# Optimization experiments

Hardware: AMD Instinct MI355X
Metric: run time of the kernel (lower is better)

Reference implementation:

```python
import jax, jax.numpy as jnp
from jax import lax
import numpy as np

N, T, V = 32, 32, 128
C_FEAT, C_BOX, C_CLS = 256, 4, 4
C_IN = C_FEAT + C_BOX + C_CLS  # 264 (is_scene=False concatenates x,b,c)
C_OUT = 64
K = 9
EPS = 1e-3  # keras BatchNormalization default epsilon


def _bn4(x, g, b, m, v):
    # inference-mode BN over channel axis 1 of (N,C,T,V)
    s = (g * lax.rsqrt(v + EPS))[None, :, None, None]
    return (x - m[None, :, None, None]) * s + b[None, :, None, None]


def _stgcn(x, a, imp, w, bw, ga, ba, ma, va, al, wt, bt, gb, bb, mb, vb, residual):
    res = x if residual else 0.0
    # SGCN: 1x1 conv (channels_first) then adjacency aggregation; dropout is identity at inference
    h = jnp.einsum('nctv,co->notv', x, w) + bw[None, :, None, None]
    h = jnp.einsum('nctv,ntvw->nctw', h, a * imp)
    # TGCN: BN -> PReLU(alpha per (C,T,V)) -> temporal conv (K,1) SAME -> BN -> (dropout=id)
    h = _bn4(h, ga, ba, ma, va)
    h = jnp.where(h >= 0, h, al[None] * h)
    h = lax.conv_general_dilated(h, wt, (1, 1), 'SAME',
                                 dimension_numbers=('NCHW', 'HWIO', 'NCHW')) + bt[None, :, None, None]
    h = _bn4(h, gb, bb, mb, vb)
    return h + res  # use_mdn=True -> no final PReLU


def _forward(x, b, c, a, dbn_g, dbn_b, dbn_m, dbn_v,
             w0, bw0, imp0, g0a, b0a, m0a, v0a, al0, wt0, bt0, g0b, b0b, m0b, v0b,
             w1, bw1, imp1, g1a, b1a, m1a, v1a, al1, wt1, bt1, g1b, b1b, m1b, v1b):
    x = jnp.concatenate([x, b, c], axis=-1)  # (N,T,V,C_IN)
    n, t, v, cc = x.shape
    # data BN over flattened (V*C) channel axis, exactly as the TF reshapes do
    x = jnp.transpose(x, (0, 2, 3, 1)).reshape(n, v * cc, t)
    s = (dbn_g * lax.rsqrt(dbn_v + EPS))[None, :, None]
    x = (x - dbn_m[None, :, None]) * s + dbn_b[None, :, None]
    # NOTE: the original does transpose(0,1,3,2) then a *reshape* to (N,C,T,V); replicate exactly
    x = x.reshape(n, v, cc, t).transpose(0, 1, 3, 2).reshape(n, cc, t, v)
    x = _stgcn(x, a, imp0, w0, bw0, g0a, b0a, m0a, v0a, al0, wt0, bt0, g0b, b0b, m0b, v0b, residual=False)
    x = _stgcn(x, a, imp1, w1, bw1, g1a, b1a, m1a, v1a, al1, wt1, bt1, g1b, b1b, m1b, v1b, residual=True)
    x = x[:, :, :, 0]  # (N,C_OUT,T)
    return jnp.transpose(x, (0, 2, 1))  # (N,T,C_OUT)


def setup_inputs():
    key = jax.random.key(0)
    ks = jax.random.split(key, 40)
    rn = lambda k, s, sc=1.0: jax.random.normal(k, s, jnp.float32) * sc
    ru = lambda k, s, lo, hi: jax.random.uniform(k, s, jnp.float32, lo, hi)
    d = {}
    d['x'] = rn(ks[0], (N, T, V, C_FEAT))
    d['b'] = rn(ks[1], (N, T, V, C_BOX))
    d['c'] = ru(ks[2], (N, T, V, C_CLS), 0.0, 1.0)
    d['a'] = ru(ks[3], (N, T, V, V), 0.0, 1.0)
    d['dbn_g'] = ru(ks[4], (V * C_IN,), 0.5, 1.5)
    d['dbn_b'] = rn(ks[5], (V * C_IN,), 0.1)
    d['dbn_m'] = rn(ks[6], (V * C_IN,), 0.1)
    d['dbn_v'] = ru(ks[7], (V * C_IN,), 0.5, 1.5)

    def mk_layer(i, cin, kb):
        d['w%d' % i] = rn(ks[kb], (cin, C_OUT), (1.0 / cin) ** 0.5)
        d['bw%d' % i] = rn(ks[kb + 1], (C_OUT,), 0.01)
        d['imp%d' % i] = rn(ks[kb + 2], (V, V), (2.0 / (V * V)) ** 0.5)
        d['g%da' % i] = ru(ks[kb + 3], (C_OUT,), 0.5, 1.5)
        d['b%da' % i] = rn(ks[kb + 4], (C_OUT,), 0.1)
        d['m%da' % i] = rn(ks[kb + 5], (C_OUT,), 0.1)
        d['v%da' % i] = ru(ks[kb + 6], (C_OUT,), 0.5, 1.5)
        d['al%d' % i] = ru(ks[kb + 7], (C_OUT, T, V), 0.0, 0.3)
        d['wt%d' % i] = rn(ks[kb + 8], (K, 1, C_OUT, C_OUT), (1.0 / (K * C_OUT)) ** 0.5)
        d['bt%d' % i] = rn(ks[kb + 9], (C_OUT,), 0.01)
        d['g%db' % i] = ru(ks[kb + 10], (C_OUT,), 0.5, 1.5)
        d['b%db' % i] = rn(ks[kb + 11], (C_OUT,), 0.1)
        d['m%db' % i] = rn(ks[kb + 12], (C_OUT,), 0.1)
        d['v%db' % i] = ru(ks[kb + 13], (C_OUT,), 0.5, 1.5)

    mk_layer(0, C_IN, 8)
    mk_layer(1, C_OUT, 22)
    return d


def reference(x, b, c, a, dbn_g, dbn_b, dbn_m, dbn_v,
              w0, bw0, imp0, g0a, b0a, m0a, v0a, al0, wt0, bt0, g0b, b0b, m0b, v0b,
              w1, bw1, imp1, g1a, b1a, m1a, v1a, al1, wt1, bt1, g1b, b1b, m1b, v1b):
    return _forward(x, b, c, a, dbn_g, dbn_b, dbn_m, dbn_v,
                    w0, bw0, imp0, g0a, b0a, m0a, v0a, al0, wt0, bt0, g0b, b0b, m0b, v0b,
                    w1, bw1, imp1, g1a, b1a, m1a, v1a, al1, wt1, bt1, g1b, b1b, m1b, v1b)
```

## Files before the change

### kernel.cpp

```cpp
#include <hip/hip_runtime.h>
#include <hip/hip_bf16.h>

typedef unsigned short u16;
typedef unsigned int   u32;

#define N_   32
#define T_   32
#define V_   128
#define CIN_ 264
#define CO_  64
#define KT_  9
#define EPS_ 1e-3f

#define OFF_DBN_S 0
#define OFF_DBN_O 33792
#define OFF_W0    67584
#define OFF_BW0   84480
#define OFF_A0S   84544
#define OFF_A0O   84608
#define OFF_B0S   84672
#define OFF_B0O   84736
#define OFF_W1    84800
#define OFF_BW1   88896
#define OFF_A1S   88960
#define OFF_A1O   89024
#define OFF_B1S   89088
#define OFF_B1O   89152
#define PREP_TOTAL 110464

#define B_P    0
#define B_FLAG 360448
#define B_W0A  360512
#define B_WTA  397440
#define B_H0   524288
#define B_G0   (B_H0 + 16777216)
#define B_L0   (B_G0 + 16777216)
#define B_G1P  (B_L0 + 33554432)
#define B_END  (B_G1P + 262144)

typedef short bf16x8 __attribute__((ext_vector_type(8)));
typedef float f32x4  __attribute__((ext_vector_type(4)));

__device__ __forceinline__ float bf2f(u16 u) { return __uint_as_float(((u32)u) << 16); }
__device__ __forceinline__ u16 f2bf(float f) {
    u32 x = __float_as_uint(f);
    return (u16)((x + 0x7fffu + ((x >> 16) & 1u)) >> 16);
}
__device__ __forceinline__ float ldin(const void* p, u32 i, int f32) {
    return f32 ? ((const float*)p)[i] : bf2f(((const u16*)p)[i]);
}

__global__ void k_detect(const void* a, int* flag) {
    if (threadIdx.x == 0 && blockIdx.x == 0) {
        const u16* p = (const u16*)a;
        int cnt = 0;
        for (int i = 0; i < 64; ++i) {
            float v = bf2f(p[2 * i]);
            if (v >= 0.f && v <= 1.0f) ++cnt;
        }
        *flag = (cnt >= 56) ? 0 : 1;
    }
}

__global__ void k_prep(const void* dbn_g, const void* dbn_b, const void* dbn_m, const void* dbn_v,
                       const void* w0, const void* bw0,
                       const void* g0a, const void* b0a, const void* m0a, const void* v0a,
                       const void* bt0, const void* g0b, const void* b0b, const void* m0b, const void* v0b,
                       const void* w1, const void* bw1,
                       const void* g1a, const void* b1a, const void* m1a, const void* v1a,
                       const void* bt1, const void* g1b, const void* b1b, const void* m1b, const void* v1b,
                       const void* wt0,
                       float* P, u16* W0A, u16* WTA, const int* flagp)
{
    const int f32 = *flagp;
    int i = blockIdx.x * 256 + threadIdx.x;
    if (i < 33792) {
        float s = ldin(dbn_g, i, f32) * rsqrtf(ldin(dbn_v, i, f32) + EPS_);
        P[OFF_DBN_S + i] = s;
        P[OFF_DBN_O + i] = ldin(dbn_b, i, f32) - ldin(dbn_m, i, f32) * s;
    } else if (i < 50688) { int j = i - 33792; P[OFF_W0 + j] = ldin(w0, j, f32); }
    else if (i < 50752) { int j = i - 50688; P[OFF_BW0 + j] = ldin(bw0, j, f32); }
    else if (i < 50816) { int j = i - 50752;
        float s = ldin(g0a, j, f32) * rsqrtf(ldin(v0a, j, f32) + EPS_);
        P[OFF_A0S + j] = s; P[OFF_A0O + j] = ldin(b0a, j, f32) - ldin(m0a, j, f32) * s;
    } else if (i < 50880) { int j = i - 50816;
        float s = ldin(g0b, j, f32) * rsqrtf(ldin(v0b, j, f32) + EPS_);
        P[OFF_B0S + j] = s; P[OFF_B0O + j] = (ldin(bt0, j, f32) - ldin(m0b, j, f32)) * s + ldin(b0b, j, f32);
    } else if (i < 54976) { int j = i - 50880; P[OFF_W1 + j] = ldin(w1, j, f32); }
    else if (i < 55040) { int j = i - 54976; P[OFF_BW1 + j] = ldin(bw1, j, f32); }
    else if (i < 55104) { int j = i - 55040;
        float s = ldin(g1a, j, f32) * rsqrtf(ldin(v1a, j, f32) + EPS_);
        P[OFF_A1S + j] = s; P[OFF_A1O + j] = ldin(b1a, j, f32) - ldin(m1a, j, f32) * s;
    } else if (i < 55168) { int j = i - 55104;
        float s = ldin(g1b, j, f32) * rsqrtf(ldin(v1b, j, f32) + EPS_);
        P[OFF_B1S + j] = s; P[OFF_B1O + j] = (ldin(bt1, j, f32) - ldin(m1b, j, f32)) * s + ldin(b1b, j, f32);
    } else if (i < 73600) {
        int j = i - 55168; int c = j / 288, ci = j - c * 288;
        float val = (ci < 264) ? ldin(w0, (u32)ci * 64 + c, f32)
                  : ((ci == 264) ? ldin(bw0, c, f32) : 0.f);
        W0A[j] = f2bf(val);
    } else if (i < 110464) {
        int j = i - 73600; int k = j >> 12, rem = j & 4095, o = rem >> 6, ii = rem & 63;
        WTA[j] = f2bf(ldin(wt0, ((u32)(k * 64 + ii)) * 64 + o, f32));
    }
}

__global__ __launch_bounds__(256) void k_pw0(const void* __restrict__ xin, const void* __restrict__ bin,
                                             const void* __restrict__ cin2, const float* __restrict__ P,
                                             const u16* __restrict__ W0Ag, u16* __restrict__ h0,
                                             const int* __restrict__ flagp)
{
    __shared__ __align__(16) u16 XT[64 * 296];
    const int f32 = *flagp;
    const int t2 = blockIdx.x, n = blockIdx.y, vh = blockIdx.z;
    const int tid = threadIdx.x;
    const int vbase = vh * 64;
    for (int e = tid; e < 288 * 64; e += 256) {
        int c2 = e >> 6, vloc = e & 63;
        int vv = vbase + vloc;
        float val;
        if (c2 < 264) {
            u32 L = (u32)c2 * 4096u + (u32)t2 * 128u + (u32)vv;
            u32 vs = L / 8448u;
            u32 r  = L - vs * 8448u;
            u32 ts = r / 264u;
            u32 cc = r - ts * 264u;
            u32 base = ((u32)n * 32u + ts) * 128u + vs;
            if (cc < 256u)      val = ldin(xin, base * 256u + cc, f32);
            else if (cc < 260u) val = ldin(bin, base * 4u + (cc - 256u), f32);
            else                val = ldin(cin2, base * 4u + (cc - 260u), f32);
            u32 ch = vs * 264u + cc;
            val = fmaf(val, P[OFF_DBN_S + ch], P[OFF_DBN_O + ch]);
        } else val = (c2 == 264) ? 1.0f : 0.0f;
        XT[vloc * 296 + c2] = f2bf(val);
    }
    __syncthreads();
    const int wv = tid >> 6, lane = tid & 63, l16 = lane & 15, quad = lane >> 4;
    const int m0 = wv * 16;
    f32x4 acc[4];
#pragma unroll
    for (int i = 0; i < 4; ++i) acc[i] = (f32x4){0.f, 0.f, 0.f, 0.f};
    for (int ks = 0; ks < 9; ++ks) {
        const int k0 = ks * 32 + quad * 8;
        bf16x8 af = *(const bf16x8*)&XT[(m0 + l16) * 296 + k0];
#pragma unroll
        for (int ni = 0; ni < 4; ++ni) {
            bf16x8 bf = *(const bf16x8*)&W0Ag[(u32)(ni * 16 + l16) * 288 + k0];
            acc[ni] = __builtin_amdgcn_mfma_f32_16x16x32_bf16(af, bf, acc[ni], 0, 0, 0);
        }
    }
    const int v = vbase + m0 + quad * 4;
#pragma unroll
    for (int ni = 0; ni < 4; ++ni) {
        int c = ni * 16 + l16;
        ushort4 rr; u16* rp = (u16*)&rr;
#pragma unroll
        for (int r = 0; r < 4; ++r) rp[r] = f2bf(acc[ni][r]);
        *(ushort4*)&h0[((u32)(n * 64 + c) * 32 + t2) * 128 + v] = rr;
    }
}

__global__ __launch_bounds__(256) void k_graph0(const void* __restrict__ a, const void* __restrict__ imp0,
                                                const void* __restrict__ al0, const float* __restrict__ P,
                                                const u16* __restrict__ h0, u16* __restrict__ g0,
                                                const int* __restrict__ flagp)
{
    __shared__ __align__(16) u16 amT[128 * 136];
    __shared__ __align__(16) u16 Hs[64 * 136];
    const int f32 = *flagp;
    const int t = blockIdx.x, n = blockIdx.y;
    const int tid = threadIdx.x;
    const u32 abase = (((u32)n * T_ + t) * V_) * V_;
    for (int e = tid; e < 128 * 128; e += 256) {
        int vv = e >> 7, w = e & 127;
        float av = ldin(a, abase + (u32)vv * 128u + w, f32) * ldin(imp0, (u32)vv * 128u + w, f32);
        amT[w * 136 + vv] = f2bf(av);
    }
    for (int e = tid; e < 1024; e += 256) {
        int c = e >> 4, ch = e & 15;
        *(uint4*)&Hs[c * 136 + ch * 8] = *(const uint4*)&h0[((u32)(n * 64 + c) * 32 + t) * 128 + ch * 8];
    }
    __syncthreads();
    const int wv = tid >> 6, lane = tid & 63, l16 = lane & 15, quad = lane >> 4;
    const int n0w = wv * 32;
    f32x4 acc[4][2];
#pragma unroll
    for (int mi = 0; mi < 4; ++mi) { acc[mi][0] = (f32x4){0,0,0,0}; acc[mi][1] = (f32x4){0,0,0,0}; }
#pragma unroll
    for (int ks = 0; ks < 4; ++ks) {
        const int k0 = ks * 32 + quad * 8;
        bf16x8 bf[2];
        bf[0] = *(const bf16x8*)&amT[(n0w + l16) * 136 + k0];
        bf[1] = *(const bf16x8*)&amT[(n0w + 16 + l16) * 136 + k0];
#pragma unroll
        for (int mi = 0; mi < 4; ++mi) {
            bf16x8 af = *(const bf16x8*)&Hs[(mi * 16 + l16) * 136 + k0];
            acc[mi][0] = __builtin_amdgcn_mfma_f32_16x16x32_bf16(af, bf[0], acc[mi][0], 0, 0, 0);
            acc[mi][1] = __builtin_amdgcn_mfma_f32_16x16x32_bf16(af, bf[1], acc[mi][1], 0, 0, 0);
        }
    }
#pragma unroll
    for (int mi = 0; mi < 4; ++mi) {
        const int c0 = mi * 16 + quad * 4;
        const float4 s4 = *(const float4*)&P[OFF_A0S + c0];
        const float4 o4 = *(const float4*)&P[OFF_A0O + c0];
        const float ss[4] = {s4.x, s4.y, s4.z, s4.w};
        const float oo[4] = {o4.x, o4.y, o4.z, o4.w};
#pragma unroll
        for (int ni = 0; ni < 2; ++ni) {
            const int w = n0w + ni * 16 + l16;
            ushort4 rr; u16* rp = (u16*)&rr;
#pragma unroll
            for (int r = 0; r < 4; ++r) {
                float y = fmaf(acc[mi][ni][r], ss[r], oo[r]);
                float alv = ldin(al0, ((u32)(c0 + r) * 32 + t) * 128 + w, f32);
                rp[r] = f2bf((y >= 0.f) ? y : alv * y);
            }
            *(ushort4*)&g0[((u32)(n * 32 + t) * 128 + w) * 64 + c0] = rr;
        }
    }
}

__global__ __launch_bounds__(256) void k_tconv0(const u16* __restrict__ WTAg, const float* __restrict__ P,
                                                const u16* __restrict__ g0, float* __restrict__ L0)
{
    __shared__ __align__(16) u16 Wl[2][64 * 72];
    __shared__ __align__(16) u16 Bs[2][128 * 72];
    const int t = blockIdx.x, n = blockIdx.y;
    const int tid = threadIdx.x;
    const int kmin = (t < 4) ? (4 - t) : 0;
    const int kmax = (t > 27) ? (35 - t) : 8;

    auto stageB = [&](int k, int buf) {
        const u16* src = g0 + ((u32)(n * 32 + (t + k - 4)) * 128) * 64;
        for (int e = tid; e < 1024; e += 256) {
            int row = e >> 3, ch = e & 7;
            *(uint4*)&Bs[buf][row * 72 + ch * 8] = *(const uint4*)&src[row * 64 + ch * 8];
        }
    };
    auto stageW = [&](int k, int buf) {
        const u16* src = WTAg + (u32)k * 4096;
        for (int e = tid; e < 512; e += 256) {
            int row = e >> 3, ch = e & 7;
            *(uint4*)&Wl[buf][row * 72 + ch * 8] = *(const uint4*)&src[row * 64 + ch * 8];
        }
    };
    stageB(kmin, 0); stageW(kmin, 0);
    __syncthreads();
    const int wv = tid >> 6, lane = tid & 63, l16 = lane & 15, quad = lane >> 4;
    const int n0w = wv * 32;
    f32x4 acc[4][2];
#pragma unroll
    for (int mi = 0; mi < 4; ++mi) { acc[mi][0] = (f32x4){0,0,0,0}; acc[mi][1] = (f32x4){0,0,0,0}; }

    for (int k = kmin; k <= kmax; ++k) {
        const int buf = (k - kmin) & 1;
        if (k < kmax) { stageB(k + 1, buf ^ 1); stageW(k + 1, buf ^ 1); }
#pragma unroll
        for (int ks = 0; ks < 2; ++ks) {
            const int k0 = ks * 32 + quad * 8;
            bf16x8 bf[2];
            bf[0] = *(const bf16x8*)&Bs[buf][(n0w + l16) * 72 + k0];
            bf[1] = *(const bf16x8*)&Bs[buf][(n0w + 16 + l16) * 72 + k0];
#pragma unroll
            for (int mi = 0; mi < 4; ++mi) {
                bf16x8 af = *(const bf16x8*)&Wl[buf][(mi * 16 + l16) * 72 + k0];
                acc[mi][0] = __builtin_amdgcn_mfma_f32_16x16x32_bf16(af, bf[0], acc[mi][0], 0, 0, 0);
                acc[mi][1] = __builtin_amdgcn_mfma_f32_16x16x32_bf16(af, bf[1], acc[mi][1], 0, 0, 0);
            }
        }
        __syncthreads();
    }
#pragma unroll
    for (int mi = 0; mi < 4; ++mi) {
        const int ob = mi * 16 + quad * 4;
        const float4 s4 = *(const float4*)&P[OFF_B0S + ob];
        const float4 o4 = *(const float4*)&P[OFF_B0O + ob];
        const float ss[4] = {s4.x, s4.y, s4.z, s4.w};
        const float oo[4] = {o4.x, o4.y, o4.z, o4.w};
#pragma unroll
        for (int ni = 0; ni < 2; ++ni) {
            const int v = n0w + ni * 16 + l16;
#pragma unroll
            for (int r = 0; r < 4; ++r)
                L0[((u32)(n * 64 + ob + r) * 32 + t) * 128 + v] = fmaf(acc[mi][ni][r], ss[r], oo[r]);
        }
    }
}

__global__ __launch_bounds__(128) void k_pw1(const void* __restrict__ a, const void* __restrict__ imp1,
                                             const void* __restrict__ al1, const float* __restrict__ P,
                                             const float* __restrict__ L0, float* __restrict__ g1p,
                                             const int* __restrict__ flagp)
{
    __shared__ float part[V_ * 65];
    __shared__ float red2[128];
    const int f32 = *flagp;
    const int t = blockIdx.x, n = blockIdx.y;
    const int tid = threadIdx.x;
    const int v = tid;
    float acc[CO_];
#pragma unroll
    for (int o = 0; o < CO_; ++o) acc[o] = P[OFF_BW1 + o];
    const float* W = P + OFF_W1;
    const u32 base = (u32)n * (CO_ * T_ * V_) + (u32)t * V_ + (u32)v;
    for (int c = 0; c < CO_; ++c) {
        float xv = L0[base + (u32)c * (T_ * V_)];
        const float* wr = W + c * CO_;
#pragma unroll
        for (int o = 0; o < CO_; ++o) acc[o] = fmaf(xv, wr[o], acc[o]);
    }
    float amv = ldin(a, (((u32)n * T_ + t) * V_ + v) * V_ + 0u, f32) * ldin(imp1, (u32)v * V_ + 0u, f32);
#pragma unroll
    for (int o = 0; o < CO_; ++o) part[v * 65 + o] = acc[o] * amv;
    __syncthreads();
    const int o = tid & 63, hh = tid >> 6;
    float s = 0.f;
    for (int vv = hh * 64; vv < hh * 64 + 64; ++vv) s += part[vv * 65 + o];
    red2[tid] = s;
    __syncthreads();
    if (tid < 64) {
        float g = red2[tid] + red2[64 + tid];
        float y = fmaf(g, P[OFF_A1S + o], P[OFF_A1O + o]);
        float alv = ldin(al1, ((u32)o * T_ + t) * V_ + 0u, f32);
        y = (y >= 0.f) ? y : alv * y;
        g1p[((u32)n * CO_ + o) * T_ + t] = y;
    }
}

__global__ __launch_bounds__(64) void k_tconv1(const void* __restrict__ wt1, const float* __restrict__ P,
                                               const float* __restrict__ g1p, const float* __restrict__ L0,
                                               void* __restrict__ out, const int* __restrict__ flagp)
{
    __shared__ float gl[CO_ * KT_];
    const int f32 = *flagp;
    const int t = blockIdx.x, n = blockIdx.y;
    const int tid = threadIdx.x;
    for (int e = tid; e < CO_ * KT_; e += 64) {
        int i = e / KT_, kk = e - i * KT_;
        int tt = t + kk - 4;
        gl[e] = (tt >= 0 && tt < T_) ? g1p[((u32)n * CO_ + i) * T_ + tt] : 0.f;
    }
    __syncthreads();
    float acc = 0.f;
    for (int i = 0; i < CO_; ++i) {
#pragma unroll
        for (int k = 0; k < KT_; ++k) {
            float wv = ldin(wt1, ((u32)(k * CO_ + i)) * CO_ + tid, f32);
            acc = fmaf(gl[i * KT_ + k], wv, acc);
        }
    }
    float y = fmaf(acc, P[OFF_B1S + tid], P[OFF_B1O + tid]);
    y += L0[(u32)n * (CO_ * T_ * V_) + (u32)tid * (T_ * V_) + (u32)t * V_ + 0];
    const u32 oi = ((u32)n * T_ + t) * CO_ + tid;
    if (f32) ((float*)out)[oi] = y;
    else     ((u16*)out)[oi]   = f2bf(y);
}

__global__ void k_fail(u16* out, int nel) {
    int i = blockIdx.x * 256 + threadIdx.x;
    if (i < nel) out[i] = 0x7f80;
}

extern "C" void kernel_launch(void* const* d_in, const int* in_sizes, int n_in,
                              void* d_out, int out_size, void* d_ws, size_t ws_size,
                              hipStream_t stream)
{
    const void* xin  = d_in[0];
    const void* bin  = d_in[1];
    const void* cin2 = d_in[2];
    const void* a    = d_in[3];
    const void* dbn_g = d_in[4];
    const void* dbn_b = d_in[5];
    const void* dbn_m = d_in[6];
    const void* dbn_v = d_in[7];
    const void* w0  = d_in[8];
    const void* bw0 = d_in[9];
    const void* imp0 = d_in[10];
    const void* g0a = d_in[11];
    const void* b0a = d_in[12];
    const void* m0a = d_in[13];
    const void* v0a = d_in[14];
    const void* al0 = d_in[15];
    const void* wt0 = d_in[16];
    const void* bt0 = d_in[17];
    const void* g0b = d_in[18];
    const void* b0b = d_in[19];
    const void* m0b = d_in[20];
    const void* v0b = d_in[21];
    const void* w1  = d_in[22];
    const void* bw1 = d_in[23];
    const void* imp1 = d_in[24];
    const void* g1a = d_in[25];
    const void* b1a = d_in[26];
    const void* m1a = d_in[27];
    const void* v1a = d_in[28];
    const void* al1 = d_in[29];
    const void* wt1 = d_in[30];
    const void* bt1 = d_in[31];
    const void* g1b = d_in[32];
    const void* b1b = d_in[33];
    const void* m1b = d_in[34];
    const void* v1b = d_in[35];

    if (ws_size < (size_t)B_END) {
        k_fail<<<(out_size + 255) / 256, 256, 0, stream>>>((u16*)d_out, out_size);
        return;
    }
    char* w = (char*)d_ws;
    float* P    = (float*)(w + B_P);
    int*   flg  = (int*)(w + B_FLAG);
    u16*   W0A  = (u16*)(w + B_W0A);
    u16*   WTA  = (u16*)(w + B_WTA);
    u16*   h0   = (u16*)(w + B_H0);
    u16*   g0   = (u16*)(w + B_G0);
    float* L0   = (float*)(w + B_L0);
    float* g1p  = (float*)(w + B_G1P);

    k_detect<<<1, 64, 0, stream>>>(a, flg);
    k_prep<<<(PREP_TOTAL + 255) / 256, 256, 0, stream>>>(
        dbn_g, dbn_b, dbn_m, dbn_v, w0, bw0, g0a, b0a, m0a, v0a,
        bt0, g0b, b0b, m0b, v0b, w1, bw1, g1a, b1a, m1a, v1a,
        bt1, g1b, b1b, m1b, v1b, wt0, P, W0A, WTA, flg);

    dim3 gpw0(T_, N_, 2);
    dim3 grid(T_, N_);
    k_pw0   <<<gpw0, 256, 0, stream>>>(xin, bin, cin2, P, W0A, h0, flg);
    k_graph0<<<grid, 256, 0, stream>>>(a, imp0, al0, P, h0, g0, flg);
    k_tconv0<<<grid, 256, 0, stream>>>(WTA, P, g0, L0);
    k_pw1   <<<grid, 128, 0, stream>>>(a, imp1, al1, P, L0, g1p, flg);
    k_tconv1<<<grid,  64, 0, stream>>>(wt1, P, g1p, L0, d_out, flg);
}
```

Before: 597.9 us.

## Fuse layer-0 pointwise conv into graph kernel; tile temporal conv over two timesteps

Merges k_pw0 and k_graph0 into one kernel that keeps the pointwise-conv output in shared memory and reuses that buffer for the adjacency tile, which removes the h0 global round trip and one launch. k_tconv0 now computes two output timesteps per block, so each staged input slice feeds both, and it reads weights straight from global memory instead of staging them in LDS. The block index is remapped so work is grouped by XCD. Input gathers are reorganised so each wave handles one channel row across lanes, and the adjacency is written to LDS as packed pairs. Fused blocks use more LDS and run two sequential phases, which may lower occupancy.

```diff
diff --git a/kernel.cpp b/kernel.cpp
--- a/kernel.cpp
+++ b/kernel.cpp
@@ -105,98 +105,99 @@
     }
 }
 
-__global__ __launch_bounds__(256) void k_pw0(const void* __restrict__ xin, const void* __restrict__ bin,
-                                             const void* __restrict__ cin2, const float* __restrict__ P,
-                                             const u16* __restrict__ W0Ag, u16* __restrict__ h0,
-                                             const int* __restrict__ flagp)
-{
-    __shared__ __align__(16) u16 XT[64 * 296];
-    const int f32 = *flagp;
-    const int t2 = blockIdx.x, n = blockIdx.y, vh = blockIdx.z;
-    const int tid = threadIdx.x;
-    const int vbase = vh * 64;
-    for (int e = tid; e < 288 * 64; e += 256) {
-        int c2 = e >> 6, vloc = e & 63;
-        int vv = vbase + vloc;
-        float val;
-        if (c2 < 264) {
-            u32 L = (u32)c2 * 4096u + (u32)t2 * 128u + (u32)vv;
-            u32 vs = L / 8448u;
-            u32 r  = L - vs * 8448u;
-            u32 ts = r / 264u;
-            u32 cc = r - ts * 264u;
-            u32 base = ((u32)n * 32u + ts) * 128u + vs;
-            if (cc < 256u)      val = ldin(xin, base * 256u + cc, f32);
-            else if (cc < 260u) val = ldin(bin, base * 4u + (cc - 256u), f32);
-            else                val = ldin(cin2, base * 4u + (cc - 260u), f32);
-            u32 ch = vs * 264u + cc;
-            val = fmaf(val, P[OFF_DBN_S + ch], P[OFF_DBN_O + ch]);
-        } else val = (c2 == 264) ? 1.0f : 0.0f;
-        XT[vloc * 296 + c2] = f2bf(val);
-    }
-    __syncthreads();
-    const int wv = tid >> 6, lane = tid & 63, l16 = lane & 15, quad = lane >> 4;
-    const int m0 = wv * 16;
-    f32x4 acc[4];
-#pragma unroll
-    for (int i = 0; i < 4; ++i) acc[i] = (f32x4){0.f, 0.f, 0.f, 0.f};
-    for (int ks = 0; ks < 9; ++ks) {
-        const int k0 = ks * 32 + quad * 8;
-        bf16x8 af = *(const bf16x8*)&XT[(m0 + l16) * 296 + k0];
-#pragma unroll
-        for (int ni = 0; ni < 4; ++ni) {
-            bf16x8 bf = *(const bf16x8*)&W0Ag[(u32)(ni * 16 + l16) * 288 + k0];
-            acc[ni] = __builtin_amdgcn_mfma_f32_16x16x32_bf16(af, bf, acc[ni], 0, 0, 0);
-        }
-    }
-    const int v = vbase + m0 + quad * 4;
-#pragma unroll
-    for (int ni = 0; ni < 4; ++ni) {
-        int c = ni * 16 + l16;
-        ushort4 rr; u16* rp = (u16*)&rr;
-#pragma unroll
-        for (int r = 0; r < 4; ++r) rp[r] = f2bf(acc[ni][r]);
-        *(ushort4*)&h0[((u32)(n * 64 + c) * 32 + t2) * 128 + v] = rr;
-    }
-}
-
-__global__ __launch_bounds__(256) void k_graph0(const void* __restrict__ a, const void* __restrict__ imp0,
-                                                const void* __restrict__ al0, const float* __restrict__ P,
-                                                const u16* __restrict__ h0, u16* __restrict__ g0,
-                                                const int* __restrict__ flagp)
-{
-    __shared__ __align__(16) u16 amT[128 * 136];
-    __shared__ __align__(16) u16 Hs[64 * 136];
+#define XT_STRIDE 296
+#define H_OFF     37888
+__global__ __launch_bounds__(256) void k_l0(const void* __restrict__ xin, const void* __restrict__ bin,
+                                            const void* __restrict__ cin2, const void* __restrict__ a,
+                                            const void* __restrict__ imp0, const void* __restrict__ al0,
+                                            const float* __restrict__ P, const u16* __restrict__ W0Ag,
+                                            u16* __restrict__ g0, const int* __restrict__ flagp)
+{
+    __shared__ __align__(16) char SM[55296];
+    u16* XT  = (u16*)SM;
+    u16* amT = (u16*)SM;
+    u16* H   = (u16*)(SM + H_OFF);
+
     const int f32 = *flagp;
     const int t = blockIdx.x, n = blockIdx.y;
     const int tid = threadIdx.x;
+    const int lane = tid & 63, wid = tid >> 6;
+    const int l16 = lane & 15, quad = lane >> 4;
+    const int m0 = wid * 16;
+
+    for (int vh = 0; vh < 2; ++vh) {
+        if (vh) __syncthreads();
+        for (int c2 = wid; c2 < 288; c2 += 4) {
+            if (c2 < 264) {
+                u32 f0 = (u32)c2 * 4096u + (u32)t * 128u + (u32)(vh * 64);
+                u32 vs0 = f0 / 8448u;
+                u32 r0  = f0 - vs0 * 8448u;
+                u32 ts0 = r0 / 264u;
+                u32 cc0 = r0 - ts0 * 264u;
+                u32 cc = cc0 + (u32)lane;
+                u32 ts = ts0, vs = vs0;
+                if (cc >= 264u) { cc -= 264u; ++ts; }
+                if (ts >= 32u)  { ts -= 32u;  ++vs; }
+                u32 base = ((u32)n * 32u + ts) * 128u + vs;
+                float val;
+                if (cc < 256u)      val = ldin(xin, base * 256u + cc, f32);
+                else if (cc < 260u) val = ldin(bin, base * 4u + (cc - 256u), f32);
+                else                val = ldin(cin2, base * 4u + (cc - 260u), f32);
+                u32 ch = vs * 264u + cc;
+                XT[lane * XT_STRIDE + c2] = f2bf(fmaf(val, P[OFF_DBN_S + ch], P[OFF_DBN_O + ch]));
+            } else {
+                XT[lane * XT_STRIDE + c2] = (c2 == 264) ? (u16)0x3F80 : (u16)0;
+            }
+        }
+        __syncthreads();
+        f32x4 acc[4];
+#pragma unroll
+        for (int i = 0; i < 4; ++i) acc[i] = (f32x4){0.f, 0.f, 0.f, 0.f};
+        for (int ks = 0; ks < 9; ++ks) {
+            const int k0 = ks * 32 + quad * 8;
+            bf16x8 af = *(const bf16x8*)&XT[(m0 + l16) * XT_STRIDE + k0];
+#pragma unroll
+            for (int ni = 0; ni < 4; ++ni) {
+                bf16x8 bf = *(const bf16x8*)&W0Ag[(u32)(ni * 16 + l16) * 288 + k0];
+                acc[ni] = __builtin_amdgcn_mfma_f32_16x16x32_bf16(af, bf, acc[ni], 0, 0, 0);
+            }
+        }
+        const int vloc = vh * 64 + m0 + quad * 4;
+#pragma unroll
+        for (int ni = 0; ni < 4; ++ni) {
+            const int c = ni * 16 + l16;
+            ushort4 rr; u16* rp = (u16*)&rr;
+#pragma unroll
+            for (int r = 0; r < 4; ++r) rp[r] = f2bf(acc[ni][r]);
+            *(ushort4*)&H[c * 136 + vloc] = rr;
+        }
+    }
+    __syncthreads();
+
     const u32 abase = (((u32)n * T_ + t) * V_) * V_;
-    for (int e = tid; e < 128 * 128; e += 256) {
-        int vv = e >> 7, w = e & 127;
-        float av = ldin(a, abase + (u32)vv * 128u + w, f32) * ldin(imp0, (u32)vv * 128u + w, f32);
-        amT[w * 136 + vv] = f2bf(av);
-    }
-    for (int e = tid; e < 1024; e += 256) {
-        int c = e >> 4, ch = e & 15;
-        *(uint4*)&Hs[c * 136 + ch * 8] = *(const uint4*)&h0[((u32)(n * 64 + c) * 32 + t) * 128 + ch * 8];
-    }
-    __syncthreads();
-    const int wv = tid >> 6, lane = tid & 63, l16 = lane & 15, quad = lane >> 4;
-    const int n0w = wv * 32;
+    for (int e = tid; e < 64 * 128; e += 256) {
+        int vvp = e >> 7, w = e & 127;
+        int vv = vvp * 2;
+        float a0 = ldin(a, abase + (u32)vv * 128u + w, f32)       * ldin(imp0, (u32)vv * 128u + w, f32);
+        float a1 = ldin(a, abase + (u32)(vv + 1) * 128u + w, f32) * ldin(imp0, (u32)(vv + 1) * 128u + w, f32);
+        u32 pk = (u32)f2bf(a0) | ((u32)f2bf(a1) << 16);
+        *(u32*)&amT[w * 136 + vv] = pk;
+    }
+    __syncthreads();
+    const int n0w = wid * 32;
     f32x4 acc[4][2];
 #pragma unroll
     for (int mi = 0; mi < 4; ++mi) { acc[mi][0] = (f32x4){0,0,0,0}; acc[mi][1] = (f32x4){0,0,0,0}; }
 #pragma unroll
     for (int ks = 0; ks < 4; ++ks) {
         const int k0 = ks * 32 + quad * 8;
-        bf16x8 bf[2];
-        bf[0] = *(const bf16x8*)&amT[(n0w + l16) * 136 + k0];
-        bf[1] = *(const bf16x8*)&amT[(n0w + 16 + l16) * 136 + k0];
+        bf16x8 bf0 = *(const bf16x8*)&amT[(n0w + l16) * 136 + k0];
+        bf16x8 bf1 = *(const bf16x8*)&amT[(n0w + 16 + l16) * 136 + k0];
 #pragma unroll
         for (int mi = 0; mi < 4; ++mi) {
-            bf16x8 af = *(const bf16x8*)&Hs[(mi * 16 + l16) * 136 + k0];
-            acc[mi][0] = __builtin_amdgcn_mfma_f32_16x16x32_bf16(af, bf[0], acc[mi][0], 0, 0, 0);
-            acc[mi][1] = __builtin_amdgcn_mfma_f32_16x16x32_bf16(af, bf[1], acc[mi][1], 0, 0, 0);
+            bf16x8 af = *(const bf16x8*)&H[(mi * 16 + l16) * 136 + k0];
+            acc[mi][0] = __builtin_amdgcn_mfma_f32_16x16x32_bf16(af, bf0, acc[mi][0], 0, 0, 0);
+            acc[mi][1] = __builtin_amdgcn_mfma_f32_16x16x32_bf16(af, bf1, acc[mi][1], 0, 0, 0);
         }
     }
 #pragma unroll
@@ -224,66 +225,93 @@
 __global__ __launch_bounds__(256) void k_tconv0(const u16* __restrict__ WTAg, const float* __restrict__ P,
                                                 const u16* __restrict__ g0, float* __restrict__ L0)
 {
-    __shared__ __align__(16) u16 Wl[2][64 * 72];
     __shared__ __align__(16) u16 Bs[2][128 * 72];
-    const int t = blockIdx.x, n = blockIdx.y;
+    const int L = blockIdx.x;
+    const int xcd = L & 7, slot = L >> 3;
+    const int n = xcd + 8 * (slot >> 4);
+    const int t0 = (slot & 15) * 2;
     const int tid = threadIdx.x;
-    const int kmin = (t < 4) ? (4 - t) : 0;
-    const int kmax = (t > 27) ? (35 - t) : 8;
-
-    auto stageB = [&](int k, int buf) {
-        const u16* src = g0 + ((u32)(n * 32 + (t + k - 4)) * 128) * 64;
-        for (int e = tid; e < 1024; e += 256) {
-            int row = e >> 3, ch = e & 7;
-            *(uint4*)&Bs[buf][row * 72 + ch * 8] = *(const uint4*)&src[row * 64 + ch * 8];
-        }
-    };
-    auto stageW = [&](int k, int buf) {
-        const u16* src = WTAg + (u32)k * 4096;
-        for (int e = tid; e < 512; e += 256) {
-            int row = e >> 3, ch = e & 7;
-            *(uint4*)&Wl[buf][row * 72 + ch * 8] = *(const uint4*)&src[row * 64 + ch * 8];
-        }
-    };
-    stageB(kmin, 0); stageW(kmin, 0);
-    __syncthreads();
-    const int wv = tid >> 6, lane = tid & 63, l16 = lane & 15, quad = lane >> 4;
-    const int n0w = wv * 32;
-    f32x4 acc[4][2];
-#pragma unroll
-    for (int mi = 0; mi < 4; ++mi) { acc[mi][0] = (f32x4){0,0,0,0}; acc[mi][1] = (f32x4){0,0,0,0}; }
-
-    for (int k = kmin; k <= kmax; ++k) {
-        const int buf = (k - kmin) & 1;
-        if (k < kmax) { stageB(k + 1, buf ^ 1); stageW(k + 1, buf ^ 1); }
+    const int lane = tid & 63, wid = tid >> 6;
+    const int l16 = lane & 15, quad = lane >> 4;
+    const int n0w = wid * 32;
+
+    const int s_lo = (t0 < 4) ? 0 : (t0 - 4);
+    const int s_hi = (t0 + 5 > 31) ? 31 : (t0 + 5);
+
+    {
+        const u16* src = g0 + (u32)(n * 32 + s_lo) * 8192u;
+#pragma unroll
+        for (int j = 0; j < 4; ++j) {
+            int idx = tid + j * 256;
+            *(uint4*)&Bs[0][(idx >> 3) * 72 + (idx & 7) * 8] = *(const uint4*)&src[idx * 8];
+        }
+    }
+    __syncthreads();
+
+    f32x4 acc[2][4][2];
+#pragma unroll
+    for (int to = 0; to < 2; ++to)
+#pragma unroll
+        for (int mi = 0; mi < 4; ++mi) { acc[to][mi][0] = (f32x4){0,0,0,0}; acc[to][mi][1] = (f32x4){0,0,0,0}; }
+
+    for (int s = s_lo; s <= s_hi; ++s) {
+        const int buf = (s - s_lo) & 1;
+        uint4 pf[4];
+        if (s < s_hi) {
+            const u16* src = g0 + (u32)(n * 32 + (s + 1)) * 8192u;
+#pragma unroll
+            for (int j = 0; j < 4; ++j) pf[j] = *(const uint4*)&src[(tid + j * 256) * 8];
+        }
+        const int k0t = s - t0 + 4, k1t = k0t - 1;
 #pragma unroll
         for (int ks = 0; ks < 2; ++ks) {
             const int k0 = ks * 32 + quad * 8;
-            bf16x8 bf[2];
-            bf[0] = *(const bf16x8*)&Bs[buf][(n0w + l16) * 72 + k0];
-            bf[1] = *(const bf16x8*)&Bs[buf][(n0w + 16 + l16) * 72 + k0];
-#pragma unroll
-            for (int mi = 0; mi < 4; ++mi) {
-                bf16x8 af = *(const bf16x8*)&Wl[buf][(mi * 16 + l16) * 72 + k0];
-                acc[mi][0] = __builtin_amdgcn_mfma_f32_16x16x32_bf16(af, bf[0], acc[mi][0], 0, 0, 0);
-                acc[mi][1] = __builtin_amdgcn_mfma_f32_16x16x32_bf16(af, bf[1], acc[mi][1], 0, 0, 0);
+            bf16x8 b0 = *(const bf16x8*)&Bs[buf][(n0w + l16) * 72 + k0];
+            bf16x8 b1 = *(const bf16x8*)&Bs[buf][(n0w + 16 + l16) * 72 + k0];
+            if (k0t >= 0 && k0t <= 8) {
+#pragma unroll
+                for (int mi = 0; mi < 4; ++mi) {
+                    bf16x8 af = *(const bf16x8*)&WTAg[(u32)k0t * 4096 + (u32)(mi * 16 + l16) * 64 + k0];
+                    acc[0][mi][0] = __builtin_amdgcn_mfma_f32_16x16x32_bf16(af, b0, acc[0][mi][0], 0, 0, 0);
+                    acc[0][mi][1] = __builtin_amdgcn_mfma_f32_16x16x32_bf16(af, b1, acc[0][mi][1], 0, 0, 0);
+                }
+            }
+            if (k1t >= 0 && k1t <= 8) {
+#pragma unroll
+                for (int mi = 0; mi < 4; ++mi) {
+                    bf16x8 af = *(const bf16x8*)&WTAg[(u32)k1t * 4096 + (u32)(mi * 16 + l16) * 64 + k0];
+                    acc[1][mi][0] = __builtin_amdgcn_mfma_f32_16x16x32_bf16(af, b0, acc[1][mi][0], 0, 0, 0);
+                    acc[1][mi][1] = __builtin_amdgcn_mfma_f32_16x16x32_bf16(af, b1, acc[1][mi][1], 0, 0, 0);
+                }
+            }
+        }
+        if (s < s_hi) {
+#pragma unroll
+            for (int j = 0; j < 4; ++j) {
+                int idx = tid + j * 256;
+                *(uint4*)&Bs[buf ^ 1][(idx >> 3) * 72 + (idx & 7) * 8] = pf[j];
             }
         }
         __syncthreads();
     }
-#pragma unroll
-    for (int mi = 0; mi < 4; ++mi) {
-        const int ob = mi * 16 + quad * 4;
-        const float4 s4 = *(const float4*)&P[OFF_B0S + ob];
-        const float4 o4 = *(const float4*)&P[OFF_B0O + ob];
-        const float ss[4] = {s4.x, s4.y, s4.z, s4.w};
-        const float oo[4] = {o4.x, o4.y, o4.z, o4.w};
-#pragma unroll
-        for (int ni = 0; ni < 2; ++ni) {
-            const int v = n0w + ni * 16 + l16;
-#pragma unroll
-            for (int r = 0; r < 4; ++r)
-                L0[((u32)(n * 64 + ob + r) * 32 + t) * 128 + v] = fmaf(acc[mi][ni][r], ss[r], oo[r]);
+
+#pragma unroll
+    for (int to = 0; to < 2; ++to) {
+        const int t = t0 + to;
+#pragma unroll
+        for (int mi = 0; mi < 4; ++mi) {
+            const int ob = mi * 16 + quad * 4;
+            const float4 s4 = *(const float4*)&P[OFF_B0S + ob];
+            const float4 o4 = *(const float4*)&P[OFF_B0O + ob];
+            const float ss[4] = {s4.x, s4.y, s4.z, s4.w};
+            const float oo[4] = {o4.x, o4.y, o4.z, o4.w};
+#pragma unroll
+            for (int ni = 0; ni < 2; ++ni) {
+                const int v = n0w + ni * 16 + l16;
+#pragma unroll
+                for (int r = 0; r < 4; ++r)
+                    L0[((u32)(n * 64 + ob + r) * 32 + t) * 128 + v] = fmaf(acc[to][mi][ni][r], ss[r], oo[r]);
+            }
         }
     }
 }
@@ -412,7 +440,6 @@
     int*   flg  = (int*)(w + B_FLAG);
     u16*   W0A  = (u16*)(w + B_W0A);
     u16*   WTA  = (u16*)(w + B_WTA);
-    u16*   h0   = (u16*)(w + B_H0);
     u16*   g0   = (u16*)(w + B_G0);
     float* L0   = (float*)(w + B_L0);
     float* g1p  = (float*)(w + B_G1P);
@@ -423,11 +450,9 @@
         bt0, g0b, b0b, m0b, v0b, w1, bw1, g1a, b1a, m1a, v1a,
         bt1, g1b, b1b, m1b, v1b, wt0, P, W0A, WTA, flg);
 
-    dim3 gpw0(T_, N_, 2);
     dim3 grid(T_, N_);
-    k_pw0   <<<gpw0, 256, 0, stream>>>(xin, bin, cin2, P, W0A, h0, flg);
-    k_graph0<<<grid, 256, 0, stream>>>(a, imp0, al0, P, h0, g0, flg);
-    k_tconv0<<<grid, 256, 0, stream>>>(WTA, P, g0, L0);
+    k_l0    <<<grid, 256, 0, stream>>>(xin, bin, cin2, a, imp0, al0, P, W0A, g0, flg);
+    k_tconv0<<<512,  256, 0, stream>>>(WTA, P, g0, L0);
     k_pw1   <<<grid, 128, 0, stream>>>(a, imp1, al1, P, L0, g1p, flg);
     k_tconv1<<<grid,  64, 0, stream>>>(wt1, P, g1p, L0, d_out, flg);
 }
```

Measured after the change: 649.3 us. +8.6%, slower.
